# Performance work log

Hardware: AMD Instinct MI355X
Metric: run time of the kernel (lower is better)

The kernel has to match this reference:

```python
import jax, jax.numpy as jnp
import numpy as np

N_HEADS = 16
EPS = 1e-5

def _ln(h, g, b):
    mu = jnp.mean(h, axis=-1, keepdims=True)
    var = jnp.var(h, axis=-1, keepdims=True)
    return (h - mu) * jax.lax.rsqrt(var + EPS) * g + b

def setup_inputs() -> dict:
    key = jax.random.key(0)
    ks = jax.random.split(key, 8)
    B, S, D, M = 2, 2048, 2048, 8192
    x = jax.random.normal(ks[0], (B, S, D), dtype=jnp.float32)
    # causal mask: True where attention is disallowed (j > i)
    mask = jnp.triu(jnp.ones((S, S), dtype=bool), k=1)[None, None]
    s = 1.0 / np.sqrt(D)
    Wq = jax.random.normal(ks[1], (D, D), dtype=jnp.float32) * s
    Wk = jax.random.normal(ks[2], (D, D), dtype=jnp.float32) * s
    Wv = jax.random.normal(ks[3], (D, D), dtype=jnp.float32) * s
    Wo = jax.random.normal(ks[4], (D, D), dtype=jnp.float32) * s
    W1 = jax.random.normal(ks[5], (D, M), dtype=jnp.float32) * s
    b1 = jnp.zeros((M,), dtype=jnp.float32)
    W2 = jax.random.normal(ks[6], (M, D), dtype=jnp.float32) * (1.0 / np.sqrt(M))
    b2 = jnp.zeros((D,), dtype=jnp.float32)
    ln1_g = jnp.ones((D,), jnp.float32); ln1_b = jnp.zeros((D,), jnp.float32)
    ln2_g = jnp.ones((D,), jnp.float32); ln2_b = jnp.zeros((D,), jnp.float32)
    return dict(x=x, self_attn_mask=mask, Wq=Wq, Wk=Wk, Wv=Wv, Wo=Wo,
                ln1_g=ln1_g, ln1_b=ln1_b, W1=W1, b1=b1, W2=W2, b2=b2,
                ln2_g=ln2_g, ln2_b=ln2_b)

def reference(x, self_attn_mask, Wq, Wk, Wv, Wo, ln1_g, ln1_b, W1, b1, W2, b2, ln2_g, ln2_b):
    B, S, D = x.shape
    n = N_HEADS
    d = D // n
    # --- self-attention with pre-norm residual ---
    h = _ln(x, ln1_g, ln1_b)
    # NOTE: source uses .view(b, n_heads, i, head_dim) with NO transpose -> plain reshape
    q = (h @ Wq).reshape(B, n, S, d)
    k = (h @ Wk).reshape(B, n, S, d)
    v = (h @ Wv).reshape(B, n, S, d)
    score = jnp.einsum('bnid,bnjd->bnij', q, k)
    # NOTE: source masks BEFORE scaling, so -1e9 is also divided by sqrt(d)
    score = jnp.where(self_attn_mask, jnp.float32(-1e9), score) / jnp.sqrt(jnp.float32(d))
    w = jax.nn.softmax(score, axis=3)
    o = jnp.einsum('bnij,bnjd->bnid', w, v)
    o = o.transpose(0, 2, 1, 3).reshape(B, S, D)  # b n i d -> b i (n d)
    x = x + o @ Wo
    # --- FFN with pre-norm residual ---
    h2 = _ln(x, ln2_g, ln2_b)
    ff = jnp.maximum(h2 @ W1 + b1, 0.0) @ W2 + b2
    return x + ff
```

## Files before the change

### kernel.cpp

```cpp
#include <hip/hip_runtime.h>
#include <cstdint>

using bf16x8 = __attribute__((ext_vector_type(8))) short;
using f32x4  = __attribute__((ext_vector_type(4))) float;

__device__ __forceinline__ unsigned short f2bf(float f) {
  union { float f; unsigned u; } v; v.f = f;
  unsigned u = v.u;
  u += 0x7fffu + ((u >> 16) & 1u);
  return (unsigned short)(u >> 16);
}

__device__ __forceinline__ void gload_lds16(const unsigned short* g, unsigned short* l) {
  __builtin_amdgcn_global_load_lds(
      (const __attribute__((address_space(1))) unsigned int*)g,
      (__attribute__((address_space(3))) unsigned int*)l, 16, 0, 0);
}

__global__ __launch_bounds__(256) void ln_kernel(
    const float* __restrict__ x, const float* __restrict__ g,
    const float* __restrict__ bb, unsigned short* __restrict__ h)
{
  const int D = 2048;
  const int row = blockIdx.x;
  const float* xr = x + (size_t)row * D;
  const int t = threadIdx.x;
  float4 v0 = ((const float4*)xr)[t];
  float4 v1 = ((const float4*)xr)[t + 256];
  float s  = v0.x+v0.y+v0.z+v0.w + v1.x+v1.y+v1.z+v1.w;
  float ss = v0.x*v0.x+v0.y*v0.y+v0.z*v0.z+v0.w*v0.w
           + v1.x*v1.x+v1.y*v1.y+v1.z*v1.z+v1.w*v1.w;
  #pragma unroll
  for (int off = 1; off < 64; off <<= 1) {
    s  += __shfl_xor(s, off);
    ss += __shfl_xor(ss, off);
  }
  __shared__ float red[8];
  const int wave = t >> 6, lane = t & 63;
  if (lane == 0) { red[wave] = s; red[4+wave] = ss; }
  __syncthreads();
  s  = red[0]+red[1]+red[2]+red[3];
  ss = red[4]+red[5]+red[6]+red[7];
  const float mu   = s * (1.f/2048.f);
  const float var  = ss * (1.f/2048.f) - mu*mu;
  const float rstd = rsqrtf(var + 1e-5f);
  unsigned short* hr = h + (size_t)row * D;
  #pragma unroll
  for (int q = 0; q < 2; ++q) {
    float4 v = q ? v1 : v0;
    int vecidx = t + q*256;
    float4 gg  = ((const float4*)g)[vecidx];
    float4 bv  = ((const float4*)bb)[vecidx];
    ushort4 o;
    o.x = f2bf((v.x-mu)*rstd*gg.x + bv.x);
    o.y = f2bf((v.y-mu)*rstd*gg.y + bv.y);
    o.z = f2bf((v.z-mu)*rstd*gg.z + bv.z);
    o.w = f2bf((v.w-mu)*rstd*gg.w + bv.w);
    *(ushort4*)(hr + vecidx*4) = o;
  }
}

__global__ __launch_bounds__(256) void transpose_cast(
    const float* __restrict__ W, unsigned short* __restrict__ WT,
    int K, int N)
{
  __shared__ float tile[32][33];
  const int tx = threadIdx.x, ty = threadIdx.y;
  const int n0 = blockIdx.x * 32, k0 = blockIdx.y * 32;
  #pragma unroll
  for (int r = 0; r < 4; ++r)
    tile[ty + r*8][tx] = W[(size_t)(k0 + ty + r*8) * N + n0 + tx];
  __syncthreads();
  #pragma unroll
  for (int r = 0; r < 4; ++r)
    WT[(size_t)(n0 + ty + r*8) * K + k0 + tx] = f2bf(tile[tx][ty + r*8]);
}

__global__ __launch_bounds__(256) void reduce_splitk(
    const float* __restrict__ P, const float* __restrict__ x2,
    const float* __restrict__ b2, float* __restrict__ out)
{
  const size_t MN4 = (size_t)4096 * 2048 / 4;
  const float4* P0 = (const float4*)P;
  const float4* P1 = P0 + MN4;
  const float4* X  = (const float4*)x2;
  const float4* B  = (const float4*)b2;
  for (size_t i = (size_t)blockIdx.x * 256 + threadIdx.x; i < MN4;
       i += (size_t)gridDim.x * 256) {
    float4 a = P0[i], b = P1[i], c = X[i], bb = B[i & 511];
    float4 o;
    o.x = a.x + b.x + c.x + bb.x;
    o.y = a.y + b.y + c.y + bb.y;
    o.z = a.z + b.z + c.z + bb.z;
    o.w = a.w + b.w + c.w + bb.w;
    ((float4*)out)[i] = o;
  }
}

template<int BM, bool BIAS, bool RELU, bool RESID, bool OUTBF16>
__global__ __launch_bounds__(512, 2) void gemm8(
    const unsigned short* __restrict__ A, const unsigned short* __restrict__ BT,
    const float* __restrict__ bias, const float* __restrict__ resid,
    void* __restrict__ Cp, int M, int N, int K, int kdepth, int nbx, int ntiles)
{
  constexpr int BN = 256, BK = 64;
  constexpr int MPH = BM / 64;
  constexpr int AQ  = BM / 64;
  constexpr int LPK = AQ + 4;
  __shared__ __align__(16) unsigned short lds[2][(BM + BN) * BK];

  const int tid  = threadIdx.x;
  const int lane = tid & 63, wave = tid >> 6;
  const int l15 = lane & 15, lh = lane >> 4;
  const int wr = wave >> 2, wc = wave & 3;

  const int nwg = gridDim.x;
  const int q8  = nwg >> 3;
  const int wg  = blockIdx.x;
  const int swz = (wg & 7) * q8 + (wg >> 3);
  const int split = swz / ntiles;
  const int tile  = swz % ntiles;
  const size_t bm = (size_t)(tile / nbx) * BM;
  const size_t bn = (size_t)(tile % nbx) * BN;
  A  += (size_t)split * kdepth;
  BT += (size_t)split * kdepth;
  const int nk = kdepth >> 6;

  auto stageA = [&](int buf, int kt, int qq) {
    int idx = qq * 512 + tid;
    int row = idx >> 3, c = idx & 7, gc = c ^ (row & 7);
    gload_lds16(A + (bm + row) * (size_t)K + (size_t)kt * BK + gc * 8,
                &lds[buf][0] + idx * 8);
  };
  auto stageB = [&](int buf, int kt, int qq) {
    int idx = qq * 512 + tid;
    int row = idx >> 3, c = idx & 7, gc = c ^ (row & 7);
    gload_lds16(BT + (bn + row) * (size_t)K + (size_t)kt * BK + gc * 8,
                &lds[buf][BM * BK] + idx * 8);
  };

  f32x4 acc[MPH * 2][4] = {};

  #pragma unroll
  for (int qq = 0; qq < AQ; ++qq) stageA(0, 0, qq);
  #pragma unroll
  for (int qq = 0; qq < 4; ++qq)  stageB(0, 0, qq);
  #pragma unroll
  for (int qq = 0; qq < AQ; ++qq) stageA(1, 1, qq);
  #pragma unroll
  for (int qq = 0; qq < 4; ++qq)  stageB(1, 1, qq);

  for (int kt = 0; kt < nk; ++kt) {
    const int buf = kt & 1;
    if (kt < nk - 1) asm volatile("s_waitcnt vmcnt(%0)" :: "i"(LPK) : "memory");
    else             asm volatile("s_waitcnt vmcnt(0)" ::: "memory");
    __builtin_amdgcn_s_barrier();
    asm volatile("" ::: "memory");

    const unsigned short* La = &lds[buf][0];
    const unsigned short* Lb = &lds[buf][BM * BK];
    bf16x8 bfr[2][4];
    const bool pf = (kt + 2 < nk);

    #pragma unroll
    for (int p = 0; p < MPH; ++p) {
      if (p == 0) {
        #pragma unroll
        for (int kk = 0; kk < 2; ++kk)
          #pragma unroll
          for (int n = 0; n < 4; ++n) {
            int brow = wc * 64 + n * 16 + l15;
            bfr[kk][n] = *(const bf16x8*)(Lb + brow * 64 +
                           ((kk * 32 + lh * 8) ^ ((brow & 7) << 3)));
          }
      }
      bf16x8 af[2][2];
      #pragma unroll
      for (int mi = 0; mi < 2; ++mi) {
        int arow = (p * 4 + wr * 2 + mi) * 16 + l15;
        #pragma unroll
        for (int kk = 0; kk < 2; ++kk)
          af[mi][kk] = *(const bf16x8*)(La + arow * 64 +
                         ((kk * 32 + lh * 8) ^ ((arow & 7) << 3)));
      }
      if (p > 0 && pf) {
        if (MPH == 4) { stageA(buf, kt + 2, p - 1); stageB(buf, kt + 2, p - 1); }
        else          { stageA(buf, kt + 2, 0);
                        stageB(buf, kt + 2, 0); stageB(buf, kt + 2, 1); }
      }
      __builtin_amdgcn_s_setprio(1);
      #pragma unroll
      for (int mi = 0; mi < 2; ++mi)
        #pragma unroll
        for (int n = 0; n < 4; ++n)
          #pragma unroll
          for (int kk = 0; kk < 2; ++kk)
            acc[p*2+mi][n] = __builtin_amdgcn_mfma_f32_16x16x32_bf16(
                af[mi][kk], bfr[kk][n], acc[p*2+mi][n], 0, 0, 0);
      __builtin_amdgcn_s_setprio(0);
      asm volatile("" ::: "memory");
      __builtin_amdgcn_s_barrier();
    }
    if (pf) {
      if (MPH == 4) { stageA(buf, kt + 2, 3); stageB(buf, kt + 2, 3); }
      else          { stageA(buf, kt + 2, 1);
                      stageB(buf, kt + 2, 2); stageB(buf, kt + 2, 3); }
    }
  }

  float bv[4];
  if (BIAS) {
    #pragma unroll
    for (int n = 0; n < 4; ++n) bv[n] = bias[bn + wc*64 + n*16 + l15];
  }
  unsigned short* Cb = (unsigned short*)Cp + (size_t)split * M * N;
  float*          Cf = (float*)Cp + (size_t)split * M * N;
  #pragma unroll
  for (int p = 0; p < MPH; ++p) {
    #pragma unroll
    for (int mi = 0; mi < 2; ++mi) {
      #pragma unroll
      for (int r = 0; r < 4; ++r) {
        size_t rrow = bm + (size_t)(p*4 + wr*2 + mi)*16 + lh*4 + r;
        #pragma unroll
        for (int n = 0; n < 4; ++n) {
          size_t ccol = bn + wc*64 + n*16 + l15;
          float v = acc[p*2+mi][n][r];
          if (BIAS)  v += bv[n];
          if (RELU)  v = fmaxf(v, 0.f);
          if (RESID) v += resid[rrow*(size_t)N + ccol];
          if (OUTBF16) Cb[rrow*(size_t)N + ccol] = f2bf(v);
          else         Cf[rrow*(size_t)N + ccol] = v;
        }
      }
    }
  }
}

__global__ __launch_bounds__(256) void attn_kernel(
    const unsigned short* __restrict__ QKV, unsigned short* __restrict__ O)
{
  constexpr float SCALE = 0.08838834764831845f;
  __shared__ __align__(16) unsigned short Kl[64*128];
  __shared__ __align__(16) unsigned short Vf[64*128];
  __shared__ __align__(16) unsigned short Pl[4*1024];
  const int bid = blockIdx.x;
  const int qt = 31 - (bid >> 5);
  const int nh = bid & 15;
  const int b  = (bid >> 4) & 1;
  const int t = threadIdx.x;
  const int lane = t & 63, wave = t >> 6;
  const int l15 = lane & 15, lh = lane >> 4;
  const int i0 = qt*64 + wave*16;
  const size_t RS = 6144;
  const size_t base = (size_t)b * 2048 * RS;

  const unsigned short* qrow = QKV + base + (size_t)(nh*128 + (i0 >> 4)) * RS;
  bf16x8 qf[4];
  #pragma unroll
  for (int c = 0; c < 4; ++c)
    qf[c] = *(const bf16x8*)(qrow + l15*128 + c*32 + lh*8);

  f32x4 of[8] = {};
  float mrun[4], lrun[4];
  #pragma unroll
  for (int r = 0; r < 4; ++r) { mrun[r] = -INFINITY; lrun[r] = 0.f; }

  const int nkt = qt + 1;
  bf16x8 kr[4], vr[4];
  auto loadKV = [&](int kt) {
    #pragma unroll
    for (int q = 0; q < 4; ++q) {
      int c = t + q*256;
      int j = c >> 4, dd0 = (c & 15) * 8;
      const size_t grow = base + (size_t)(nh*128 + kt*4 + (j >> 4)) * RS + (j & 15)*128 + dd0;
      kr[q] = *(const bf16x8*)(QKV + grow + 2048);
      vr[q] = *(const bf16x8*)(QKV + grow + 4096);
    }
  };
  loadKV(0);

  for (int kt = 0; kt < nkt; ++kt) {
    __syncthreads();
    #pragma unroll
    for (int q = 0; q < 4; ++q) {
      int c = t + q*256;
      int j = c >> 4, dd0 = (c & 15) * 8;
      *(bf16x8*)((char*)Kl + ((j*256 + dd0*2) ^ ((j & 7) << 4))) = kr[q];
      int ks = j >> 5, jq = j & 31;
      int cc = dd0 >> 4;
      int wb = ks*8192 + cc*1024 + (((dd0 & 15) + 16*((jq >> 3) & 3)) & ~7)*16 + (jq & 7)*2;
      #pragma unroll
      for (int e = 0; e < 8; ++e)
        *(unsigned short*)((char*)Vf + wb + ((e ^ cc) * 16)) = (unsigned short)vr[q][e];
    }
    __syncthreads();
    if (kt + 1 < nkt) loadKV(kt + 1);

    f32x4 sc[4] = {};
    #pragma unroll
    for (int jt = 0; jt < 4; ++jt) {
      int row = jt*16 + l15;
      const char* kb = (const char*)Kl + row*256;
      const int sw = (row & 7) << 4;
      #pragma unroll
      for (int c = 0; c < 4; ++c) {
        bf16x8 kf = *(const bf16x8*)(kb + ((c*64 + lh*16) ^ sw));
        sc[jt] = __builtin_amdgcn_mfma_f32_16x16x32_bf16(qf[c], kf, sc[jt], 0, 0, 0);
      }
    }

    float fac[4];
    char* pw = (char*)Pl + wave*2048;
    #pragma unroll
    for (int r = 0; r < 4; ++r) {
      float s0 = sc[0][r]*SCALE, s1 = sc[1][r]*SCALE, s2 = sc[2][r]*SCALE, s3 = sc[3][r]*SCALE;
      if (kt == qt) {
        const int i = i0 + lh*4 + r;
        const int j = kt*64 + l15;
        s0 = (j      > i) ? -INFINITY : s0;
        s1 = (j + 16 > i) ? -INFINITY : s1;
        s2 = (j + 32 > i) ? -INFINITY : s2;
        s3 = (j + 48 > i) ? -INFINITY : s3;
      }
      float mx = fmaxf(fmaxf(s0, s1), fmaxf(s2, s3));
      #pragma unroll
      for (int mk = 1; mk < 16; mk <<= 1) mx = fmaxf(mx, __shfl_xor(mx, mk));
      const float mnew = fmaxf(mrun[r], mx);
      float p0 = __expf(s0 - mnew), p1 = __expf(s1 - mnew);
      float p2 = __expf(s2 - mnew), p3 = __expf(s3 - mnew);
      float psum = (p0 + p1) + (p2 + p3);
      #pragma unroll
      for (int mk = 1; mk < 16; mk <<= 1) psum += __shfl_xor(psum, mk);
      fac[r]  = __expf(mrun[r] - mnew);
      lrun[r] = lrun[r]*fac[r] + psum;
      mrun[r] = mnew;
      const int io = lh*4 + r;
      const int swp = (io & 7) << 4;
      char* pr = pw + io*128;
      *(unsigned short*)(pr + ((     l15*2) ^ swp)) = f2bf(p0);
      *(unsigned short*)(pr + ((32 + l15*2) ^ swp)) = f2bf(p1);
      *(unsigned short*)(pr + ((64 + l15*2) ^ swp)) = f2bf(p2);
      *(unsigned short*)(pr + ((96 + l15*2) ^ swp)) = f2bf(p3);
    }
    #pragma unroll
    for (int c = 0; c < 8; ++c)
      #pragma unroll
      for (int r = 0; r < 4; ++r)
        of[c][r] *= fac[r];

    const char* prd = pw + l15*128;
    const int psw = (l15 & 7) << 4;
    bf16x8 pa0 = *(const bf16x8*)(prd + ((     lh*16) ^ psw));
    bf16x8 pa1 = *(const bf16x8*)(prd + ((64 + lh*16) ^ psw));

    #pragma unroll
    for (int c = 0; c < 8; ++c) {
      const char* vb = (const char*)Vf + c*1024 + ((lane ^ c) * 16);
      bf16x8 v0 = *(const bf16x8*)(vb);
      bf16x8 v1 = *(const bf16x8*)(vb + 8192);
      of[c] = __builtin_amdgcn_mfma_f32_16x16x32_bf16(pa0, v0, of[c], 0, 0, 0);
      of[c] = __builtin_amdgcn_mfma_f32_16x16x32_bf16(pa1, v1, of[c], 0, 0, 0);
    }
  }

  unsigned short* orow = O + ((size_t)(b*2048 + i0))*2048 + nh*128;
  #pragma unroll
  for (int r = 0; r < 4; ++r) {
    const float inv = 1.f / lrun[r];
    #pragma unroll
    for (int c = 0; c < 8; ++c)
      orow[(size_t)(lh*4 + r)*2048 + c*16 + l15] = f2bf(of[c][r]*inv);
  }
}

extern "C" void kernel_launch(void* const* d_in, const int* in_sizes, int n_in,
                              void* d_out, int out_size, void* d_ws, size_t ws_size,
                              hipStream_t stream)
{
  const float* x    = (const float*)d_in[0];
  const float* Wq   = (const float*)d_in[2];
  const float* Wk   = (const float*)d_in[3];
  const float* Wv   = (const float*)d_in[4];
  const float* Wo   = (const float*)d_in[5];
  const float* ln1g = (const float*)d_in[6];
  const float* ln1b = (const float*)d_in[7];
  const float* W1   = (const float*)d_in[8];
  const float* b1   = (const float*)d_in[9];
  const float* W2   = (const float*)d_in[10];
  const float* b2   = (const float*)d_in[11];
  const float* ln2g = (const float*)d_in[12];
  const float* ln2b = (const float*)d_in[13];
  float* out = (float*)d_out;

  char* ws = (char*)d_ws;
  unsigned short* WqkvT  = (unsigned short*)(ws);
  unsigned short* WoT    = (unsigned short*)(ws + 25165824);
  unsigned short* W1T    = (unsigned short*)(ws + 33554432);
  unsigned short* W2T    = (unsigned short*)(ws + 67108864);
  unsigned short* h      = (unsigned short*)(ws + 100663296);
  float*          x2     = (float*)(ws + 117440512);
  unsigned short* QKV    = (unsigned short*)(ws + 150994944);
  unsigned short* attn_o = (unsigned short*)(ws + 201326592);
  unsigned short* ff1    = (unsigned short*)(ws + 150994944);
  float*          Pws    = (float*)(ws);

  dim3 tb(32, 8);
  transpose_cast<<<dim3(64, 64),  tb, 0, stream>>>(Wq, WqkvT,                2048, 2048);
  transpose_cast<<<dim3(64, 64),  tb, 0, stream>>>(Wk, WqkvT + 2048*2048,    2048, 2048);
  transpose_cast<<<dim3(64, 64),  tb, 0, stream>>>(Wv, WqkvT + 2*2048*2048,  2048, 2048);
  transpose_cast<<<dim3(64, 64),  tb, 0, stream>>>(Wo, WoT,                  2048, 2048);
  transpose_cast<<<dim3(256, 64), tb, 0, stream>>>(W1, W1T,                  2048, 8192);
  transpose_cast<<<dim3(64, 256), tb, 0, stream>>>(W2, W2T,                  8192, 2048);

  ln_kernel<<<4096, 256, 0, stream>>>(x, ln1g, ln1b, h);
  gemm8<256,false,false,false,true><<<384, 512, 0, stream>>>(
      h, WqkvT, nullptr, nullptr, QKV, 4096, 6144, 2048, 2048, 24, 384);
  attn_kernel<<<1024, 256, 0, stream>>>(QKV, attn_o);
  gemm8<128,false,false,true,false><<<256, 512, 0, stream>>>(
      attn_o, WoT, nullptr, x, x2, 4096, 2048, 2048, 2048, 8, 256);
  ln_kernel<<<4096, 256, 0, stream>>>(x2, ln2g, ln2b, h);
  gemm8<256,true,true,false,true><<<512, 512, 0, stream>>>(
      h, W1T, b1, nullptr, ff1, 4096, 8192, 2048, 2048, 32, 512);
  gemm8<256,false,false,false,false><<<256, 512, 0, stream>>>(
      ff1, W2T, nullptr, nullptr, Pws, 4096, 2048, 8192, 4096, 8, 128);
  reduce_splitk<<<2048, 256, 0, stream>>>(Pws, x2, b2, out);
}
```

Before: 628.7 us.

## Software-pipeline GEMM LDS reads across k-steps and store split-K partials as bf16

Replaces the GEMM main loop with a fixed 256x256 tile whose A/B fragments for the next k-step are read from LDS during the current step's MFMA clusters. Global-to-LDS prefetches are spread across four phases. The Wo projection switches from a 128-row tile to a 2-way split-K with a separate reduce kernel. Split-K partials for both Wo and W2 are now written in bf16 instead of fp32 to cut partial-sum traffic, at the cost of accuracy in the partial sums and one extra kernel launch.

```diff
diff --git a/kernel.cpp b/kernel.cpp
--- a/kernel.cpp
+++ b/kernel.cpp
@@ -9,6 +9,9 @@
   unsigned u = v.u;
   u += 0x7fffu + ((u >> 16) & 1u);
   return (unsigned short)(u >> 16);
+}
+__device__ __forceinline__ float bf2f(unsigned short s) {
+  union { unsigned u; float f; } v; v.u = ((unsigned)s) << 16; return v.f;
 }
 
 __device__ __forceinline__ void gload_lds16(const unsigned short* g, unsigned short* l) {
@@ -76,37 +79,44 @@
     WT[(size_t)(n0 + ty + r*8) * K + k0 + tx] = f2bf(tile[tx][ty + r*8]);
 }
 
+template<bool BIAS>
 __global__ __launch_bounds__(256) void reduce_splitk(
-    const float* __restrict__ P, const float* __restrict__ x2,
-    const float* __restrict__ b2, float* __restrict__ out)
-{
-  const size_t MN4 = (size_t)4096 * 2048 / 4;
-  const float4* P0 = (const float4*)P;
-  const float4* P1 = P0 + MN4;
-  const float4* X  = (const float4*)x2;
-  const float4* B  = (const float4*)b2;
-  for (size_t i = (size_t)blockIdx.x * 256 + threadIdx.x; i < MN4;
+    const unsigned short* __restrict__ P, const float* __restrict__ resid,
+    const float* __restrict__ bias, float* __restrict__ out)
+{
+  const size_t MN8 = (size_t)4096 * 2048 / 8;
+  for (size_t i = (size_t)blockIdx.x * 256 + threadIdx.x; i < MN8;
        i += (size_t)gridDim.x * 256) {
-    float4 a = P0[i], b = P1[i], c = X[i], bb = B[i & 511];
-    float4 o;
-    o.x = a.x + b.x + c.x + bb.x;
-    o.y = a.y + b.y + c.y + bb.y;
-    o.z = a.z + b.z + c.z + bb.z;
-    o.w = a.w + b.w + c.w + bb.w;
-    ((float4*)out)[i] = o;
-  }
-}
-
-template<int BM, bool BIAS, bool RELU, bool RESID, bool OUTBF16>
-__global__ __launch_bounds__(512, 2) void gemm8(
+    bf16x8 p0 = ((const bf16x8*)P)[i];
+    bf16x8 p1 = ((const bf16x8*)P)[i + MN8];
+    float4 r0 = ((const float4*)resid)[i*2];
+    float4 r1 = ((const float4*)resid)[i*2 + 1];
+    float4 b0 = {}, b1 = {};
+    if (BIAS) {
+      b0 = ((const float4*)bias)[(i & 255) * 2];
+      b1 = ((const float4*)bias)[(i & 255) * 2 + 1];
+    }
+    float4 o0, o1;
+    o0.x = bf2f((unsigned short)p0[0]) + bf2f((unsigned short)p1[0]) + r0.x + b0.x;
+    o0.y = bf2f((unsigned short)p0[1]) + bf2f((unsigned short)p1[1]) + r0.y + b0.y;
+    o0.z = bf2f((unsigned short)p0[2]) + bf2f((unsigned short)p1[2]) + r0.z + b0.z;
+    o0.w = bf2f((unsigned short)p0[3]) + bf2f((unsigned short)p1[3]) + r0.w + b0.w;
+    o1.x = bf2f((unsigned short)p0[4]) + bf2f((unsigned short)p1[4]) + r1.x + b1.x;
+    o1.y = bf2f((unsigned short)p0[5]) + bf2f((unsigned short)p1[5]) + r1.y + b1.y;
+    o1.z = bf2f((unsigned short)p0[6]) + bf2f((unsigned short)p1[6]) + r1.z + b1.z;
+    o1.w = bf2f((unsigned short)p0[7]) + bf2f((unsigned short)p1[7]) + r1.w + b1.w;
+    ((float4*)out)[i*2]     = o0;
+    ((float4*)out)[i*2 + 1] = o1;
+  }
+}
+
+template<bool BIAS, bool RELU, bool RESID, bool OUTBF16>
+__global__ __launch_bounds__(512, 2) void gemm9(
     const unsigned short* __restrict__ A, const unsigned short* __restrict__ BT,
     const float* __restrict__ bias, const float* __restrict__ resid,
     void* __restrict__ Cp, int M, int N, int K, int kdepth, int nbx, int ntiles)
 {
-  constexpr int BN = 256, BK = 64;
-  constexpr int MPH = BM / 64;
-  constexpr int AQ  = BM / 64;
-  constexpr int LPK = AQ + 4;
+  constexpr int BM = 256, BN = 256, BK = 64;
   __shared__ __align__(16) unsigned short lds[2][(BM + BN) * BK];
 
   const int tid  = threadIdx.x;
@@ -114,9 +124,7 @@
   const int l15 = lane & 15, lh = lane >> 4;
   const int wr = wave >> 2, wc = wave & 3;
 
-  const int nwg = gridDim.x;
-  const int q8  = nwg >> 3;
-  const int wg  = blockIdx.x;
+  const int nwg = gridDim.x, q8 = nwg >> 3, wg = blockIdx.x;
   const int swz = (wg & 7) * q8 + (wg >> 3);
   const int split = swz / ntiles;
   const int tile  = swz % ntiles;
@@ -126,87 +134,104 @@
   BT += (size_t)split * kdepth;
   const int nk = kdepth >> 6;
 
-  auto stageA = [&](int buf, int kt, int qq) {
-    int idx = qq * 512 + tid;
-    int row = idx >> 3, c = idx & 7, gc = c ^ (row & 7);
-    gload_lds16(A + (bm + row) * (size_t)K + (size_t)kt * BK + gc * 8,
-                &lds[buf][0] + idx * 8);
+  const int srow = tid >> 3;
+  const int sc   = (tid & 7) ^ (srow & 7);
+  const unsigned short* aSrc = A  + (bm + srow) * (size_t)K + sc * 8;
+  const unsigned short* bSrc = BT + (bn + srow) * (size_t)K + sc * 8;
+  const size_t qStride = (size_t)64 * K;
+
+  const int aswz = (l15 & 7) << 4;
+  const int rx0 = (lh * 16) ^ aswz;
+  const int rx1 = (64 + lh * 16) ^ aswz;
+  char* const lbase = (char*)&lds[0][0];
+
+  bf16x8 af[4][2][2];
+  bf16x8 bfr[2][4];
+  f32x4  acc[8][4] = {};
+
+  auto stA = [&](int buf, int kt2, int qq) {
+    gload_lds16(aSrc + (size_t)kt2 * BK + qq * qStride,
+                &lds[buf][qq * 4096 + tid * 8]);
   };
-  auto stageB = [&](int buf, int kt, int qq) {
-    int idx = qq * 512 + tid;
-    int row = idx >> 3, c = idx & 7, gc = c ^ (row & 7);
-    gload_lds16(BT + (bn + row) * (size_t)K + (size_t)kt * BK + gc * 8,
-                &lds[buf][BM * BK] + idx * 8);
+  auto stB = [&](int buf, int kt2, int qq) {
+    gload_lds16(bSrc + (size_t)kt2 * BK + qq * qStride,
+                &lds[buf][BM * BK + qq * 4096 + tid * 8]);
   };
-
-  f32x4 acc[MPH * 2][4] = {};
-
-  #pragma unroll
-  for (int qq = 0; qq < AQ; ++qq) stageA(0, 0, qq);
-  #pragma unroll
-  for (int qq = 0; qq < 4; ++qq)  stageB(0, 0, qq);
-  #pragma unroll
-  for (int qq = 0; qq < AQ; ++qq) stageA(1, 1, qq);
-  #pragma unroll
-  for (int qq = 0; qq < 4; ++qq)  stageB(1, 1, qq);
+  auto rdA4 = [&](int buf, int q, int slot) {
+    const char* p = lbase + buf * 65536 + (wr*32 + l15) * 128 + q * 8192;
+    #pragma unroll
+    for (int mi = 0; mi < 2; ++mi) {
+      af[slot][mi][0] = *(const bf16x8*)(p + mi*2048 + rx0);
+      af[slot][mi][1] = *(const bf16x8*)(p + mi*2048 + rx1);
+    }
+  };
+  auto rdB8 = [&](int buf) {
+    const char* p = lbase + buf * 65536 + 32768 + (wc*64 + l15) * 128;
+    #pragma unroll
+    for (int n = 0; n < 4; ++n) {
+      bfr[0][n] = *(const bf16x8*)(p + n*2048 + rx0);
+      bfr[1][n] = *(const bf16x8*)(p + n*2048 + rx1);
+    }
+  };
+
+#define CLUSTER(P)                                                         \
+  __builtin_amdgcn_s_setprio(1);                                           \
+  { _Pragma("unroll")                                                      \
+    for (int mi = 0; mi < 2; ++mi)                                         \
+      { _Pragma("unroll")                                                  \
+        for (int n = 0; n < 4; ++n)                                        \
+          { _Pragma("unroll")                                              \
+            for (int kk = 0; kk < 2; ++kk)                                 \
+              acc[(P)*2+mi][n] = __builtin_amdgcn_mfma_f32_16x16x32_bf16(  \
+                  af[P][mi][kk], bfr[kk][n], acc[(P)*2+mi][n], 0, 0, 0);   \
+          } } }                                                            \
+  __builtin_amdgcn_s_setprio(0);
+#define BAR() asm volatile("" ::: "memory"); __builtin_amdgcn_s_barrier(); \
+              asm volatile("" ::: "memory")
+
+  #pragma unroll
+  for (int qq = 0; qq < 4; ++qq) stB(0, 0, qq);
+  #pragma unroll
+  for (int qq = 0; qq < 4; ++qq) stA(0, 0, qq);
+  #pragma unroll
+  for (int qq = 0; qq < 4; ++qq) stB(1, 1, qq);
+  #pragma unroll
+  for (int qq = 0; qq < 4; ++qq) stA(1, 1, qq);
+  asm volatile("s_waitcnt vmcnt(1)" ::: "memory");
+  BAR();
+  rdA4(0, 0, 0); rdA4(0, 1, 1); rdB8(0);
+  BAR();
 
   for (int kt = 0; kt < nk; ++kt) {
-    const int buf = kt & 1;
-    if (kt < nk - 1) asm volatile("s_waitcnt vmcnt(%0)" :: "i"(LPK) : "memory");
-    else             asm volatile("s_waitcnt vmcnt(0)" ::: "memory");
-    __builtin_amdgcn_s_barrier();
-    asm volatile("" ::: "memory");
-
-    const unsigned short* La = &lds[buf][0];
-    const unsigned short* Lb = &lds[buf][BM * BK];
-    bf16x8 bfr[2][4];
+    const int buf = kt & 1, nb = buf ^ 1;
+    const bool hasNext = (kt + 1 < nk);
     const bool pf = (kt + 2 < nk);
-
-    #pragma unroll
-    for (int p = 0; p < MPH; ++p) {
-      if (p == 0) {
-        #pragma unroll
-        for (int kk = 0; kk < 2; ++kk)
-          #pragma unroll
-          for (int n = 0; n < 4; ++n) {
-            int brow = wc * 64 + n * 16 + l15;
-            bfr[kk][n] = *(const bf16x8*)(Lb + brow * 64 +
-                           ((kk * 32 + lh * 8) ^ ((brow & 7) << 3)));
-          }
-      }
-      bf16x8 af[2][2];
-      #pragma unroll
-      for (int mi = 0; mi < 2; ++mi) {
-        int arow = (p * 4 + wr * 2 + mi) * 16 + l15;
-        #pragma unroll
-        for (int kk = 0; kk < 2; ++kk)
-          af[mi][kk] = *(const bf16x8*)(La + arow * 64 +
-                         ((kk * 32 + lh * 8) ^ ((arow & 7) << 3)));
-      }
-      if (p > 0 && pf) {
-        if (MPH == 4) { stageA(buf, kt + 2, p - 1); stageB(buf, kt + 2, p - 1); }
-        else          { stageA(buf, kt + 2, 0);
-                        stageB(buf, kt + 2, 0); stageB(buf, kt + 2, 1); }
-      }
-      __builtin_amdgcn_s_setprio(1);
-      #pragma unroll
-      for (int mi = 0; mi < 2; ++mi)
-        #pragma unroll
-        for (int n = 0; n < 4; ++n)
-          #pragma unroll
-          for (int kk = 0; kk < 2; ++kk)
-            acc[p*2+mi][n] = __builtin_amdgcn_mfma_f32_16x16x32_bf16(
-                af[mi][kk], bfr[kk][n], acc[p*2+mi][n], 0, 0, 0);
-      __builtin_amdgcn_s_setprio(0);
-      asm volatile("" ::: "memory");
-      __builtin_amdgcn_s_barrier();
-    }
-    if (pf) {
-      if (MPH == 4) { stageA(buf, kt + 2, 3); stageB(buf, kt + 2, 3); }
-      else          { stageA(buf, kt + 2, 1);
-                      stageB(buf, kt + 2, 2); stageB(buf, kt + 2, 3); }
-    }
-  }
+    if (kt > 0) {
+      asm volatile("s_waitcnt vmcnt(1)" ::: "memory");
+      BAR();
+    }
+    if (pf) { stB(buf, kt+2, 0); stB(buf, kt+2, 1); stA(buf, kt+2, 0); }
+    rdA4(buf, 2, 2);
+    __builtin_amdgcn_sched_barrier(0);
+    CLUSTER(0);
+    BAR();
+    if (pf) { stB(buf, kt+2, 2); stB(buf, kt+2, 3); stA(buf, kt+2, 1); stA(buf, kt+2, 2); }
+    rdA4(buf, 3, 3);
+    __builtin_amdgcn_sched_barrier(0);
+    CLUSTER(1);
+    BAR();
+    if (pf) { stA(buf, kt+2, 3); }
+    if (hasNext) rdA4(nb, 0, 0);
+    __builtin_amdgcn_sched_barrier(0);
+    CLUSTER(2);
+    BAR();
+    if (hasNext) rdA4(nb, 1, 1);
+    __builtin_amdgcn_sched_barrier(0);
+    CLUSTER(3);
+    if (hasNext) rdB8(nb);
+  }
+#undef CLUSTER
+#undef BAR
 
   float bv[4];
   if (BIAS) {
@@ -216,7 +241,7 @@
   unsigned short* Cb = (unsigned short*)Cp + (size_t)split * M * N;
   float*          Cf = (float*)Cp + (size_t)split * M * N;
   #pragma unroll
-  for (int p = 0; p < MPH; ++p) {
+  for (int p = 0; p < 4; ++p) {
     #pragma unroll
     for (int mi = 0; mi < 2; ++mi) {
       #pragma unroll
@@ -403,7 +428,8 @@
   unsigned short* QKV    = (unsigned short*)(ws + 150994944);
   unsigned short* attn_o = (unsigned short*)(ws + 201326592);
   unsigned short* ff1    = (unsigned short*)(ws + 150994944);
-  float*          Pws    = (float*)(ws);
+  unsigned short* Pwo    = (unsigned short*)(ws + 150994944);
+  unsigned short* Pw2    = (unsigned short*)(ws);
 
   dim3 tb(32, 8);
   transpose_cast<<<dim3(64, 64),  tb, 0, stream>>>(Wq, WqkvT,                2048, 2048);
@@ -414,15 +440,16 @@
   transpose_cast<<<dim3(64, 256), tb, 0, stream>>>(W2, W2T,                  8192, 2048);
 
   ln_kernel<<<4096, 256, 0, stream>>>(x, ln1g, ln1b, h);
-  gemm8<256,false,false,false,true><<<384, 512, 0, stream>>>(
+  gemm9<false,false,false,true><<<384, 512, 0, stream>>>(
       h, WqkvT, nullptr, nullptr, QKV, 4096, 6144, 2048, 2048, 24, 384);
   attn_kernel<<<1024, 256, 0, stream>>>(QKV, attn_o);
-  gemm8<128,false,false,true,false><<<256, 512, 0, stream>>>(
-      attn_o, WoT, nullptr, x, x2, 4096, 2048, 2048, 2048, 8, 256);
+  gemm9<false,false,false,true><<<256, 512, 0, stream>>>(
+      attn_o, WoT, nullptr, nullptr, Pwo, 4096, 2048, 2048, 1024, 8, 128);
+  reduce_splitk<false><<<2048, 256, 0, stream>>>(Pwo, x, nullptr, x2);
   ln_kernel<<<4096, 256, 0, stream>>>(x2, ln2g, ln2b, h);
-  gemm8<256,true,true,false,true><<<512, 512, 0, stream>>>(
+  gemm9<true,true,false,true><<<512, 512, 0, stream>>>(
       h, W1T, b1, nullptr, ff1, 4096, 8192, 2048, 2048, 32, 512);
-  gemm8<256,false,false,false,false><<<256, 512, 0, stream>>>(
-      ff1, W2T, nullptr, nullptr, Pws, 4096, 2048, 8192, 4096, 8, 128);
-  reduce_splitk<<<2048, 256, 0, stream>>>(Pws, x2, b2, out);
-}
+  gemm9<false,false,false,true><<<256, 512, 0, stream>>>(
+      ff1, W2T, nullptr, nullptr, Pw2, 4096, 2048, 8192, 4096, 8, 128);
+  reduce_splitk<true><<<2048, 256, 0, stream>>>(Pw2, x2, b2, out);
+}
```

After: 624.3 us. Within noise of the previous version (-0.7%).
